# Optimization experiments

Hardware: AMD Instinct MI355X
Metric: run time of the kernel (lower is better)

## Reference

```python
import jax, jax.numpy as jnp
import numpy as np

# ---- fixed problem dimensions ----
B, S, T = 64, 200, 32          # batch of sequences, trees per seq, nodes per tree
V, E, C = 50000, 128, 128      # vocab, embedding_dim, encode_dim
H, OUT = 100, 104              # GRU hidden, output_dim
N = B * S * T                  # total nodes
D_MAX = 5                      # max depth of a 32-node complete binary tree


def setup_inputs() -> dict:
    key = jax.random.key(0)
    ks = jax.random.split(key, 16)
    # --- tree structure: every tree is a complete binary tree with T nodes ---
    local_parent = np.array([0] + [(i - 1) // 2 for i in range(1, T)], dtype=np.int64)
    local_depth = np.array([int(np.floor(np.log2(i + 1))) for i in range(T)], dtype=np.int64)
    num_trees = B * S
    offsets = np.arange(num_trees, dtype=np.int64) * T
    node_parent = (offsets[:, None] + local_parent[None, :]).reshape(-1)
    node_depth = np.tile(local_depth, num_trees)
    node_tree = np.repeat(np.arange(num_trees, dtype=np.int64), T)
    node_tokens = jax.random.randint(ks[0], (N,), 0, V, dtype=jnp.int64)
    sc = 0.05
    inp = {
        "node_tokens": node_tokens,
        "node_parent": jnp.asarray(node_parent),
        "node_tree": jnp.asarray(node_tree),
        "node_depth": jnp.asarray(node_depth),
        "emb": jax.random.normal(ks[1], (V, E), jnp.float32) * sc,
        "w_lin": jax.random.normal(ks[2], (C, E), jnp.float32) * sc,
        "b_lin": jnp.zeros((C,), jnp.float32),
        "w_ih_f": jax.random.normal(ks[3], (3 * H, C), jnp.float32) * sc,
        "w_hh_f": jax.random.normal(ks[4], (3 * H, H), jnp.float32) * sc,
        "b_ih_f": jnp.zeros((3 * H,), jnp.float32),
        "b_hh_f": jnp.zeros((3 * H,), jnp.float32),
        "w_ih_b": jax.random.normal(ks[5], (3 * H, C), jnp.float32) * sc,
        "w_hh_b": jax.random.normal(ks[6], (3 * H, H), jnp.float32) * sc,
        "b_ih_b": jnp.zeros((3 * H,), jnp.float32),
        "b_hh_b": jnp.zeros((3 * H,), jnp.float32),
        "fc_w": jax.random.normal(ks[7], (OUT, 2 * H), jnp.float32) * sc,
        "fc_b": jnp.zeros((OUT,), jnp.float32),
    }
    return inp


def _gru(x_sbc, w_ih, w_hh, b_ih, b_hh):
    """Torch-convention GRU over leading time axis. x_sbc: [S, B, C] -> [S, B, H]."""
    h0 = jnp.zeros((x_sbc.shape[1], w_hh.shape[1]), x_sbc.dtype)

    def step(h, xt):
        gx = xt @ w_ih.T + b_ih
        gh = h @ w_hh.T + b_hh
        xr, xz, xn = jnp.split(gx, 3, axis=-1)
        hr, hz, hn = jnp.split(gh, 3, axis=-1)
        r = jax.nn.sigmoid(xr + hr)
        z = jax.nn.sigmoid(xz + hz)
        n = jnp.tanh(xn + r * hn)
        h_new = (1.0 - z) * n + z * h
        return h_new, h_new

    _, hs = jax.lax.scan(step, h0, x_sbc)
    return hs


def reference(node_tokens, node_parent, node_tree, node_depth,
              emb, w_lin, b_lin,
              w_ih_f, w_hh_f, b_ih_f, b_hh_f,
              w_ih_b, w_hh_b, b_ih_b, b_hh_b,
              fc_w, fc_b):
    # per-node contribution: W * emb(token) + b   (recursion base of hidden_state)
    c = emb[node_tokens] @ w_lin.T + b_lin               # [N, C]
    # level-batched bottom-up scatter-add: h(node) = c(node) + sum(h(children))
    h = c
    for d in range(D_MAX, 0, -1):
        mask = (node_depth == d)[:, None]
        h = h.at[node_parent].add(jnp.where(mask, h, 0.0))
    # per-tree max pool over all node hidden states (TreeEncoder output)
    tree_vec = jax.ops.segment_max(h, node_tree, num_segments=B * S)  # [B*S, C]
    x = tree_vec.reshape(B, S, C)
    # bidirectional GRU (batch_first in torch; scan over time here)
    x_t = jnp.transpose(x, (1, 0, 2))                    # [S, B, C]
    fwd = _gru(x_t, w_ih_f, w_hh_f, b_ih_f, b_hh_f)      # [S, B, H]
    bwd = _gru(x_t[::-1], w_ih_b, w_hh_b, b_ih_b, b_hh_b)[::-1]
    gru_out = jnp.concatenate([fwd, bwd], axis=-1)       # [S, B, 2H]
    pool = gru_out.max(axis=0)                           # [B, 2H] (max over time)
    return pool @ fc_w.T + fc_b                          # [B, OUT]
```

## Files before the change

kernel.cpp:

```cpp
#include <hip/hip_runtime.h>
#include <hip/hip_bf16.h>
#include <math.h>

#define BB 64
#define SS 200
#define TT 32
#define EE 128
#define CC 128
#define HH 100
#define G3 300
#define OUTD 104
#define NTREE (BB*SS)

typedef __attribute__((ext_vector_type(4))) float f32x4;
typedef _Float16 f16x8 __attribute__((ext_vector_type(8)));

__device__ inline float fast_sigmoid(float x) {
    return __builtin_amdgcn_rcpf(1.f + __builtin_amdgcn_exp2f(-1.4426950408889634f * x));
}
__device__ inline float fast_tanh(float x) {
    return 1.f - 2.f * __builtin_amdgcn_rcpf(1.f + __builtin_amdgcn_exp2f(2.8853900817779268f * x));
}
__device__ inline unsigned pack2f16(float a, float b) {
    union { _Float16 h[2]; unsigned u; } x;
    x.h[0] = (_Float16)a; x.h[1] = (_Float16)b;
    return x.u;
}
__device__ inline float subtree_cnt(int p) {
    return (p == 0) ? 32.f : (p == 1) ? 16.f : (p == 2) ? 15.f :
           (p == 3) ? 8.f  : (p <= 6) ? 7.f  : (p == 7) ? 4.f  :
           (p <= 14) ? 3.f : (p == 15) ? 2.f : 1.f;
}

#define BAR() asm volatile("s_waitcnt lgkmcnt(0)\n\ts_barrier" ::: "memory")


__global__ __launch_bounds__(256) void k0_prep(const float* __restrict__ w_lin,
                                               const float* __restrict__ w_ih_f,
                                               const float* __restrict__ w_ih_b,
                                               _Float16* __restrict__ wl,
                                               _Float16* __restrict__ k2b) {
    const int tid  = threadIdx.x;
    const int wave = tid >> 6;
    const int lane = tid & 63;
    const int r = lane & 15;
    const int q = lane >> 4;
    if (blockIdx.x == 0) {
#pragma unroll
        for (int nt = 0; nt < 2; ++nt)
#pragma unroll
            for (int kt = 0; kt < 4; ++kt) {
                const int n = wave * 32 + nt * 16 + r;
                const float* src = w_lin + (long)n * EE + kt * 32 + q * 8;
                f16x8 f;
#pragma unroll
                for (int e = 0; e < 8; ++e) f[e] = (_Float16)src[e];
                *(f16x8*)&wl[(size_t)((((wave * 2 + nt) * 4 + kt) * 64) + lane) * 8] = f;
            }
    } else {
        const int nb = blockIdx.x - 1;
        const int n = nb * 64 + wave * 16 + r;
        const int dir = (n >= 320) ? 1 : 0;
        const int j = n - dir * 320;
        const int jj = (j < G3) ? j : 0;
        const float* w = dir ? w_ih_b : w_ih_f;
#pragma unroll
        for (int kt = 0; kt < 4; ++kt) {
            const float* src = w + (long)jj * EE + kt * 32 + q * 8;
            f16x8 f;
#pragma unroll
            for (int e = 0; e < 8; ++e) f[e] = (_Float16)src[e];
            *(f16x8*)&k2b[(size_t)((((nb * 4 + wave) * 4 + kt) * 64) + lane) * 8] = f;
        }
    }
}

#define LDA 136
__global__ __launch_bounds__(512, 4) void k1_mfma(const int* __restrict__ tok,
                                                  const float* __restrict__ emb,
                                                  const _Float16* __restrict__ wl,
                                                  const float* __restrict__ b_lin,
                                                  _Float16* __restrict__ thi) {
    __shared__ __align__(16) _Float16 A_sh[64 * LDA];
    __shared__ int tok_sh[64];

    const int tid  = threadIdx.x;
    const int wave = tid >> 6;
    const int lane = tid & 63;
    const int r = lane & 15;
    const int q = lane >> 4;

    f16x8 bfrag[4];
#pragma unroll
    for (int kt = 0; kt < 4; ++kt)
        bfrag[kt] = *(const f16x8*)&wl[(size_t)(((wave * 4 + kt) * 64) + lane) * 8];
    const float bias = b_lin[wave * 16 + r];

    f16x8 l2f[2];
#pragma unroll
    for (int mt2 = 0; mt2 < 2; ++mt2) {
        const int p = mt2 * 16 + r;
#pragma unroll
        for (int e = 0; e < 8; ++e) {
            int x = q * 8 + e;
            while (x > p) x = (x - 1) >> 1;
            l2f[mt2][e] = (_Float16)((x == p) ? 1.f : 0.f);
        }
    }

    const int tree0 = blockIdx.x * 2;
    if (tid < 64) tok_sh[tid] = tok[tree0 * TT + tid];
    __syncthreads();

#pragma unroll
    for (int i = 0; i < 2; ++i) {
        const int idx = tid + i * 512;
        const int row = idx >> 4;
        const int p4  = idx & 15;
        const float4* src = (const float4*)(emb + (long)tok_sh[row] * EE + p4 * 8);
        const float4 e0 = src[0], e1 = src[1];
        f16x8 v;
        v[0] = (_Float16)e0.x; v[1] = (_Float16)e0.y; v[2] = (_Float16)e0.z; v[3] = (_Float16)e0.w;
        v[4] = (_Float16)e1.x; v[5] = (_Float16)e1.y; v[6] = (_Float16)e1.z; v[7] = (_Float16)e1.w;
        *(f16x8*)&A_sh[row * LDA + p4 * 8] = v;
    }
    __syncthreads();

    unsigned pk[4][2];
#pragma unroll
    for (int mt = 0; mt < 4; ++mt) {
        const int m = mt * 16 + r;
        f32x4 acc = (f32x4)(0.f);
#pragma unroll
        for (int kt = 0; kt < 4; ++kt) {
            f16x8 af = *(const f16x8*)&A_sh[m * LDA + kt * 32 + q * 8];
            acc = __builtin_amdgcn_mfma_f32_16x16x32_f16(af, bfrag[kt], acc, 0, 0, 0);
        }
        pk[mt][0] = pack2f16(acc[0], acc[1]);
        pk[mt][1] = pack2f16(acc[2], acc[3]);
    }

#pragma unroll
    for (int t = 0; t < 2; ++t) {
        const int l0 = (r + 16 * ((2 * q) & 3)) << 2;
        const int l1 = (r + 16 * ((2 * q + 1) & 3)) << 2;
        const bool hi = (q >> 1) != 0;
        const unsigned x0 = __builtin_amdgcn_ds_bpermute(l0, (int)pk[2 * t][0]);
        const unsigned y0 = __builtin_amdgcn_ds_bpermute(l0, (int)pk[2 * t + 1][0]);
        const unsigned x1 = __builtin_amdgcn_ds_bpermute(l0, (int)pk[2 * t][1]);
        const unsigned y1 = __builtin_amdgcn_ds_bpermute(l0, (int)pk[2 * t + 1][1]);
        const unsigned x2 = __builtin_amdgcn_ds_bpermute(l1, (int)pk[2 * t][0]);
        const unsigned y2 = __builtin_amdgcn_ds_bpermute(l1, (int)pk[2 * t + 1][0]);
        const unsigned x3 = __builtin_amdgcn_ds_bpermute(l1, (int)pk[2 * t][1]);
        const unsigned y3 = __builtin_amdgcn_ds_bpermute(l1, (int)pk[2 * t + 1][1]);
        union { unsigned u[4]; f16x8 v; } b2;
        b2.u[0] = hi ? y0 : x0;
        b2.u[1] = hi ? y1 : x1;
        b2.u[2] = hi ? y2 : x2;
        b2.u[3] = hi ? y3 : x3;

        float mx = -1e30f;
#pragma unroll
        for (int mt2 = 0; mt2 < 2; ++mt2) {
            f32x4 a2 = __builtin_amdgcn_mfma_f32_16x16x32_f16(l2f[mt2], b2.v, (f32x4)(0.f), 0, 0, 0);
#pragma unroll
            for (int reg = 0; reg < 4; ++reg) {
                const int p = mt2 * 16 + q * 4 + reg;
                mx = fmaxf(mx, a2[reg] + subtree_cnt(p) * bias);
            }
        }
        mx = fmaxf(mx, __shfl_xor(mx, 16, 64));
        mx = fmaxf(mx, __shfl_xor(mx, 32, 64));
        if (q == 0)
            thi[(size_t)(tree0 + t) * CC + wave * 16 + r] = (_Float16)mx;
    }
}

__global__ __launch_bounds__(256) void k2_mfma(const _Float16* __restrict__ thi,
                                               const _Float16* __restrict__ k2b,
                                               const float* __restrict__ b_ih_f,
                                               const float* __restrict__ b_ih_b,
                                               float* __restrict__ gx) {
    __shared__ __align__(16) _Float16 Ah[32 * LDA];

    const int tid  = threadIdx.x;
    const int wave = tid >> 6;
    const int lane = tid & 63;
    const int r = lane & 15;
    const int q = lane >> 4;

    const int nb = blockIdx.x % 10;
    const int mb = blockIdx.x / 10;
    const int m0 = mb * 32;
    const int n0 = nb * 64;

#pragma unroll
    for (int i = 0; i < 2; ++i) {
        const int idx = tid + i * 256;
        const int row = idx >> 4;
        const int p   = idx & 15;
        f16x8 v = *(const f16x8*)&thi[(size_t)(m0 + row) * CC + p * 8];
        *(f16x8*)&Ah[row * LDA + p * 8] = v;
    }
    f16x8 bh[4];
#pragma unroll
    for (int kt = 0; kt < 4; ++kt)
        bh[kt] = *(const f16x8*)&k2b[(size_t)((((nb * 4 + wave) * 4 + kt) * 64) + lane) * 8];
    __syncthreads();

    f32x4 acc[2];
    acc[0] = (f32x4)(0.f); acc[1] = (f32x4)(0.f);
#pragma unroll
    for (int mt = 0; mt < 2; ++mt) {
        const int m = mt * 16 + r;
#pragma unroll
        for (int kt = 0; kt < 4; ++kt) {
            f16x8 a = *(const f16x8*)&Ah[m * LDA + kt * 32 + q * 8];
            acc[mt] = __builtin_amdgcn_mfma_f32_16x16x32_f16(a, bh[kt], acc[mt], 0, 0, 0);
        }
    }

    const int ng  = n0 + wave * 16 + r;
    const int dir = (ng >= 320) ? 1 : 0;
    const int j   = ng - dir * 320;
    const bool valid = (j < G3);
    const float bias = valid ? (dir ? b_ih_b[j] : b_ih_f[j]) : 0.f;
    float* gxd = gx + (long)dir * NTREE * G3;
    if (valid) {
#pragma unroll
        for (int mt = 0; mt < 2; ++mt)
#pragma unroll
            for (int reg = 0; reg < 4; ++reg) {
                const int m = m0 + mt * 16 + q * 4 + reg;
                gxd[(long)m * G3 + j] = acc[mt][reg] + bias;
            }
    }
}

__global__ __launch_bounds__(256, 1) void k3_gru(const float* __restrict__ gx,
                                                 const float* __restrict__ w_hh_f,
                                                 const float* __restrict__ b_hh_f,
                                                 const float* __restrict__ w_hh_b,
                                                 const float* __restrict__ b_hh_b,
                                                 float* __restrict__ pool) {
    const int bid = blockIdx.x;
    const int dir = bid & 1;
    const int b = bid >> 1;
    const float* w_hh = dir ? w_hh_b : w_hh_f;
    const float* b_hh = dir ? b_hh_b : b_hh_f;

    __shared__ __align__(16) _Float16 h_sh[2][128];
    __shared__ float g_sh[4][80];

    const int tid  = threadIdx.x;
    const int wave = tid >> 6;
    const int lane = tid & 63;
    const int r = lane & 15;
    const int q = lane >> 4;

    f16x8 bf[5][4];
#pragma unroll
    for (int i = 0; i < 5; ++i) {
        const int l = i * 16 + r;
        const int gate = l / 25;
        const int ch   = l - gate * 25;
        const bool nv  = (l < 75);
        const int row  = gate * HH + wave * 25 + ch;
#pragma unroll
        for (int kt = 0; kt < 4; ++kt) {
            f16x8 f;
#pragma unroll
            for (int e = 0; e < 8; ++e) {
                const int k = kt * 32 + q * 8 + e;
                f[e] = (_Float16)((nv && k < HH) ? w_hh[row * HH + k] : 0.f);
            }
            bf[i][kt] = f;
        }
    }

    const int m = lane;
    const int c = wave * 25 + m;
    const bool act = (m < 25);
    float br = 0.f, bz = 0.f, bn = 0.f;
    if (act) { br = b_hh[c]; bz = b_hh[HH + c]; bn = b_hh[2 * HH + c]; }

    if (tid < 128) { h_sh[0][tid] = (_Float16)0.f; h_sh[1][tid] = (_Float16)0.f; }

    const float* gxd = gx + (long)dir * NTREE * G3;
    const int sstep = dir ? -1 : 1;
    int s = dir ? (SS - 1) : 0;
    float xr = 0.f, xz = 0.f, xn = 0.f;
    if (act) {
        const float* row0 = gxd + ((long)b * SS + s) * G3;
        xr = row0[c]; xz = row0[HH + c]; xn = row0[2 * HH + c];
    }
    float hj = 0.f, hmax = -1e30f;
    __syncthreads();

    for (int t = 0; t < SS; ++t) {
        const int p = t & 1;
        const int s_n = s + sstep;
        float xrn = 0.f, xzn = 0.f, xnn = 0.f;
        if (act && t < SS - 1) {
            const float* row0 = gxd + ((long)b * SS + s_n) * G3;
            xrn = row0[c]; xzn = row0[HH + c]; xnn = row0[2 * HH + c];
        }

        f16x8 a[4];
#pragma unroll
        for (int kt = 0; kt < 4; ++kt)
            a[kt] = *(const f16x8*)&h_sh[p][kt * 32 + q * 8];
        f32x4 acc[5];
#pragma unroll
        for (int i = 0; i < 5; ++i) {
            acc[i] = (f32x4)(0.f);
#pragma unroll
            for (int kt = 0; kt < 4; ++kt)
                acc[i] = __builtin_amdgcn_mfma_f32_16x16x32_f16(a[kt], bf[i][kt], acc[i], 0, 0, 0);
        }
        if (q == 0) {
#pragma unroll
            for (int i = 0; i < 5; ++i)
                g_sh[wave][i * 16 + r] = acc[i][0];
        }
        if (act) {
            const float ghr = g_sh[wave][m];
            const float ghz = g_sh[wave][25 + m];
            const float ghn = g_sh[wave][50 + m];
            const float rg = fast_sigmoid(xr + ghr + br);
            const float zg = fast_sigmoid(xz + ghz + bz);
            const float ng = fast_tanh(xn + rg * (ghn + bn));
            hj = (1.f - zg) * ng + zg * hj;
            hmax = fmaxf(hmax, hj);
            h_sh[1 - p][c] = (_Float16)hj;
            xr = xrn; xz = xzn; xn = xnn;
        }
        BAR();
        s = s_n;
    }
    if (act) pool[(long)b * (2 * HH) + dir * HH + c] = hmax;
}

__global__ __launch_bounds__(256) void k4_fc(const float* __restrict__ pool,
                                             const float* __restrict__ fc_w,
                                             const float* __restrict__ fc_b,
                                             float* __restrict__ out) {
    const int b = blockIdx.x;
    __shared__ __align__(16) float p_sh[2 * HH];
    const int t = threadIdx.x;
    if (t < 2 * HH) p_sh[t] = pool[(long)b * (2 * HH) + t];
    __syncthreads();
    if (t < OUTD) {
        const float4* wr4 = (const float4*)(fc_w + (long)t * (2 * HH));
        const float4* p4 = (const float4*)p_sh;
        float a0 = 0.f, a1 = 0.f;
#pragma unroll
        for (int k = 0; k < 50; k += 2) {
            float4 w0 = wr4[k],   p0 = p4[k];
            float4 w1 = wr4[k+1], p1 = p4[k+1];
            a0 += w0.x*p0.x + w0.y*p0.y + w0.z*p0.z + w0.w*p0.w;
            a1 += w1.x*p1.x + w1.y*p1.y + w1.z*p1.z + w1.w*p1.w;
        }
        out[(long)b * OUTD + t] = fc_b[t] + a0 + a1;
    }
}

extern "C" void kernel_launch(void* const* d_in, const int* in_sizes, int n_in,
                              void* d_out, int out_size, void* d_ws, size_t ws_size,
                              hipStream_t stream) {
    const int*   tok    = (const int*)d_in[0];
    const float* emb    = (const float*)d_in[4];
    const float* w_lin  = (const float*)d_in[5];
    const float* b_lin  = (const float*)d_in[6];
    const float* w_ih_f = (const float*)d_in[7];
    const float* w_hh_f = (const float*)d_in[8];
    const float* b_ih_f = (const float*)d_in[9];
    const float* b_hh_f = (const float*)d_in[10];
    const float* w_ih_b = (const float*)d_in[11];
    const float* w_hh_b = (const float*)d_in[12];
    const float* b_ih_b = (const float*)d_in[13];
    const float* b_hh_b = (const float*)d_in[14];
    const float* fc_w   = (const float*)d_in[15];
    const float* fc_b   = (const float*)d_in[16];

    char* wsb = (char*)d_ws;
    _Float16* wl   = (_Float16*)(wsb);
    _Float16* k2b  = (_Float16*)(wsb + 32768);
    _Float16* thi  = (_Float16*)(wsb + 196608);
    float*    gx   = (float*)(wsb + 3473408);
    float*    pool = (float*)(wsb);
    float*    out  = (float*)d_out;

    k0_prep<<<11, 256, 0, stream>>>(w_lin, w_ih_f, w_ih_b, wl, k2b);
    k1_mfma<<<NTREE / 2, 512, 0, stream>>>(tok, emb, wl, b_lin, thi);
    k2_mfma<<<(NTREE / 32) * 10, 256, 0, stream>>>(thi, k2b, b_ih_f, b_ih_b, gx);
    k3_gru <<<2 * BB, 256, 0, stream>>>(gx, w_hh_f, b_hh_f, w_hh_b, b_hh_b, pool);
    k4_fc  <<<BB, 256, 0, stream>>>(pool, fc_w, fc_b, out);
}
```

Baseline: 257.8 us.

## Pre-convert embedding table to fp16 and use bpermute in GRU step

```diff
diff --git a/kernel.cpp b/kernel.cpp
--- a/kernel.cpp
+++ b/kernel.cpp
@@ -11,6 +11,7 @@
 #define G3 300
 #define OUTD 104
 #define NTREE (BB*SS)
+#define EMB_N (50000 * EE)
 
 typedef __attribute__((ext_vector_type(4))) float f32x4;
 typedef _Float16 f16x8 __attribute__((ext_vector_type(8)));
@@ -26,6 +27,8 @@
     x.h[0] = (_Float16)a; x.h[1] = (_Float16)b;
     return x.u;
 }
+__device__ inline unsigned f2u(float v) { union { float f; unsigned u; } x; x.f = v; return x.u; }
+__device__ inline float u2f(unsigned v) { union { unsigned u; float f; } x; x.u = v; return x.f; }
 __device__ inline float subtree_cnt(int p) {
     return (p == 0) ? 32.f : (p == 1) ? 16.f : (p == 2) ? 15.f :
            (p == 3) ? 8.f  : (p <= 6) ? 7.f  : (p == 7) ? 4.f  :
@@ -38,8 +41,10 @@
 __global__ __launch_bounds__(256) void k0_prep(const float* __restrict__ w_lin,
                                                const float* __restrict__ w_ih_f,
                                                const float* __restrict__ w_ih_b,
+                                               const float* __restrict__ emb,
                                                _Float16* __restrict__ wl,
-                                               _Float16* __restrict__ k2b) {
+                                               _Float16* __restrict__ k2b,
+                                               _Float16* __restrict__ emb16) {
     const int tid  = threadIdx.x;
     const int wave = tid >> 6;
     const int lane = tid & 63;
@@ -57,7 +62,7 @@
                 for (int e = 0; e < 8; ++e) f[e] = (_Float16)src[e];
                 *(f16x8*)&wl[(size_t)((((wave * 2 + nt) * 4 + kt) * 64) + lane) * 8] = f;
             }
-    } else {
+    } else if (blockIdx.x <= 10) {
         const int nb = blockIdx.x - 1;
         const int n = nb * 64 + wave * 16 + r;
         const int dir = (n >= 320) ? 1 : 0;
@@ -72,12 +77,26 @@
             for (int e = 0; e < 8; ++e) f[e] = (_Float16)src[e];
             *(f16x8*)&k2b[(size_t)((((nb * 4 + wave) * 4 + kt) * 64) + lane) * 8] = f;
         }
+    } else {
+        const long base = (long)(blockIdx.x - 11) * 8192;
+#pragma unroll
+        for (int i = 0; i < 4; ++i) {
+            const long off = base + i * 2048 + tid * 8;
+            if (off < EMB_N) {
+                const float4 e0 = ((const float4*)(emb + off))[0];
+                const float4 e1 = ((const float4*)(emb + off))[1];
+                f16x8 v;
+                v[0] = (_Float16)e0.x; v[1] = (_Float16)e0.y; v[2] = (_Float16)e0.z; v[3] = (_Float16)e0.w;
+                v[4] = (_Float16)e1.x; v[5] = (_Float16)e1.y; v[6] = (_Float16)e1.z; v[7] = (_Float16)e1.w;
+                *(f16x8*)&emb16[off] = v;
+            }
+        }
     }
 }
 
 #define LDA 136
 __global__ __launch_bounds__(512, 4) void k1_mfma(const int* __restrict__ tok,
-                                                  const float* __restrict__ emb,
+                                                  const _Float16* __restrict__ emb16,
                                                   const _Float16* __restrict__ wl,
                                                   const float* __restrict__ b_lin,
                                                   _Float16* __restrict__ thi) {
@@ -117,11 +136,7 @@
         const int idx = tid + i * 512;
         const int row = idx >> 4;
         const int p4  = idx & 15;
-        const float4* src = (const float4*)(emb + (long)tok_sh[row] * EE + p4 * 8);
-        const float4 e0 = src[0], e1 = src[1];
-        f16x8 v;
-        v[0] = (_Float16)e0.x; v[1] = (_Float16)e0.y; v[2] = (_Float16)e0.z; v[3] = (_Float16)e0.w;
-        v[4] = (_Float16)e1.x; v[5] = (_Float16)e1.y; v[6] = (_Float16)e1.z; v[7] = (_Float16)e1.w;
+        f16x8 v = *(const f16x8*)&emb16[(size_t)tok_sh[row] * EE + p4 * 8];
         *(f16x8*)&A_sh[row * LDA + p4 * 8] = v;
     }
     __syncthreads();
@@ -250,7 +265,6 @@
     const float* b_hh = dir ? b_hh_b : b_hh_f;
 
     __shared__ __align__(16) _Float16 h_sh[2][128];
-    __shared__ float g_sh[4][80];
 
     const int tid  = threadIdx.x;
     const int wave = tid >> 6;
@@ -295,6 +309,8 @@
         xr = row0[c]; xz = row0[HH + c]; xn = row0[2 * HH + c];
     }
     float hj = 0.f, hmax = -1e30f;
+    const int lz = ((25 + m) & 15) << 2;
+    const int ln = ((50 + m) & 15) << 2;
     __syncthreads();
 
     for (int t = 0; t < SS; ++t) {
@@ -310,23 +326,26 @@
 #pragma unroll
         for (int kt = 0; kt < 4; ++kt)
             a[kt] = *(const f16x8*)&h_sh[p][kt * 32 + q * 8];
-        f32x4 acc[5];
+        float g[5];
 #pragma unroll
         for (int i = 0; i < 5; ++i) {
-            acc[i] = (f32x4)(0.f);
-#pragma unroll
-            for (int kt = 0; kt < 4; ++kt)
-                acc[i] = __builtin_amdgcn_mfma_f32_16x16x32_f16(a[kt], bf[i][kt], acc[i], 0, 0, 0);
-        }
-        if (q == 0) {
-#pragma unroll
-            for (int i = 0; i < 5; ++i)
-                g_sh[wave][i * 16 + r] = acc[i][0];
-        }
+            f32x4 a0 = __builtin_amdgcn_mfma_f32_16x16x32_f16(a[0], bf[i][0], (f32x4)(0.f), 0, 0, 0);
+            a0       = __builtin_amdgcn_mfma_f32_16x16x32_f16(a[1], bf[i][1], a0, 0, 0, 0);
+            f32x4 a1 = __builtin_amdgcn_mfma_f32_16x16x32_f16(a[2], bf[i][2], (f32x4)(0.f), 0, 0, 0);
+            a1       = __builtin_amdgcn_mfma_f32_16x16x32_f16(a[3], bf[i][3], a1, 0, 0, 0);
+            g[i] = a0[0] + a1[0];
+        }
+
+        const unsigned bz1 = __builtin_amdgcn_ds_bpermute(lz, (int)f2u(g[1]));
+        const unsigned bz2 = __builtin_amdgcn_ds_bpermute(lz, (int)f2u(g[2]));
+        const unsigned bz3 = __builtin_amdgcn_ds_bpermute(lz, (int)f2u(g[3]));
+        const unsigned bn3 = __builtin_amdgcn_ds_bpermute(ln, (int)f2u(g[3]));
+        const unsigned bn4 = __builtin_amdgcn_ds_bpermute(ln, (int)f2u(g[4]));
+
         if (act) {
-            const float ghr = g_sh[wave][m];
-            const float ghz = g_sh[wave][25 + m];
-            const float ghn = g_sh[wave][50 + m];
+            const float ghr = (m < 16) ? g[0] : g[1];
+            const float ghz = (m < 7) ? u2f(bz1) : (m < 23) ? u2f(bz2) : u2f(bz3);
+            const float ghn = (m < 14) ? u2f(bn3) : u2f(bn4);
             const float rg = fast_sigmoid(xr + ghr + br);
             const float zg = fast_sigmoid(xz + ghz + bz);
             const float ng = fast_tanh(xn + rg * (ghn + bn));
@@ -384,15 +403,16 @@
     const float* fc_b   = (const float*)d_in[16];
 
     char* wsb = (char*)d_ws;
-    _Float16* wl   = (_Float16*)(wsb);
-    _Float16* k2b  = (_Float16*)(wsb + 32768);
-    _Float16* thi  = (_Float16*)(wsb + 196608);
-    float*    gx   = (float*)(wsb + 3473408);
-    float*    pool = (float*)(wsb);
-    float*    out  = (float*)d_out;
-
-    k0_prep<<<11, 256, 0, stream>>>(w_lin, w_ih_f, w_ih_b, wl, k2b);
-    k1_mfma<<<NTREE / 2, 512, 0, stream>>>(tok, emb, wl, b_lin, thi);
+    _Float16* wl    = (_Float16*)(wsb);
+    _Float16* k2b   = (_Float16*)(wsb + 32768);
+    _Float16* thi   = (_Float16*)(wsb + 196608);
+    float*    gx    = (float*)(wsb + 3473408);
+    _Float16* emb16 = (_Float16*)(wsb + 3473408);
+    float*    pool  = (float*)(wsb);
+    float*    out   = (float*)d_out;
+
+    k0_prep<<<11 + 782, 256, 0, stream>>>(w_lin, w_ih_f, w_ih_b, emb, wl, k2b, emb16);
+    k1_mfma<<<NTREE / 2, 512, 0, stream>>>(tok, emb16, wl, b_lin, thi);
     k2_mfma<<<(NTREE / 32) * 10, 256, 0, stream>>>(thi, k2b, b_ih_f, b_ih_b, gx);
     k3_gru <<<2 * BB, 256, 0, stream>>>(gx, w_hh_f, b_hh_f, w_hh_b, b_hh_b, pool);
     k4_fc  <<<BB, 256, 0, stream>>>(pool, fc_w, fc_b, out);
```

Measured after the change: 252.9 us. No clear change (-1.9%).
